# Optimization experiments

Measured on AMD Instinct MI355X. Metric: run time of the kernel, lower is better.

## Reference

```python
import jax, jax.numpy as jnp
import numpy as np

PSP_SIZES = (1, 3, 6, 8)
EPS = 1e-5  # BatchNorm eps (torch default)


def _adaptive_max_pool_flat(x, s):
    # Faithful torch AdaptiveMaxPool2d: window i is [floor(i*H/s), ceil((i+1)*H/s)).
    B, C, H, W = x.shape
    hs = [int(np.floor(i * H / s)) for i in range(s)]
    he = [int(np.ceil((i + 1) * H / s)) for i in range(s)]
    ws = [int(np.floor(j * W / s)) for j in range(s)]
    we = [int(np.ceil((j + 1) * W / s)) for j in range(s)]
    cells = []
    for i in range(s):  # small static loop (s <= 8)
        for j in range(s):
            cells.append(jnp.max(x[:, :, hs[i]:he[i], ws[j]:we[j]], axis=(2, 3)))
    return jnp.stack(cells, axis=-1)  # [B, C, s*s]


def _psp(x):
    return jnp.concatenate([_adaptive_max_pool_flat(x, s) for s in PSP_SIZES], axis=-1)  # [B, C, 110]


def _conv1x1(x, w):
    # x: [B, Cin, H, W], w: [Cout, Cin]
    return jnp.einsum('bchw,oc->bohw', x, w)


def _bn(y, gamma, beta, mean, var):
    inv = jax.lax.rsqrt(var + EPS)
    return (y - mean[None, :, None, None]) * (gamma * inv)[None, :, None, None] + beta[None, :, None, None]


def setup_inputs() -> dict:
    key = jax.random.key(0)
    ks = jax.random.split(key, 4)
    B, Cin, H, W = 8, 512, 64, 64
    Ck, Cv = 256, 512
    x = jax.random.normal(ks[0], (B, Cin, H, W), dtype=jnp.float32)
    qk_w = jax.random.normal(ks[1], (Ck, Cin), dtype=jnp.float32) * 0.02
    v_w = jax.random.normal(ks[2], (Cv, Cin), dtype=jnp.float32) * 0.02
    out_w = jax.random.normal(ks[3], (Cin, Cv), dtype=jnp.float32) * 0.02
    return {
        'x': x,
        'qk_w': qk_w, 'qk_gamma': jnp.ones(Ck), 'qk_beta': jnp.zeros(Ck),
        'qk_mean': jnp.zeros(Ck), 'qk_var': jnp.ones(Ck),
        'v_w': v_w, 'v_gamma': jnp.ones(Cv), 'v_beta': jnp.zeros(Cv),
        'v_mean': jnp.zeros(Cv), 'v_var': jnp.ones(Cv),
        'out_w': out_w, 'out_gamma': jnp.ones(Cin), 'out_beta': jnp.zeros(Cin),
        'out_mean': jnp.zeros(Cin), 'out_var': jnp.ones(Cin),
    }


def reference(x, qk_w, qk_gamma, qk_beta, qk_mean, qk_var,
              v_w, v_gamma, v_beta, v_mean, v_var,
              out_w, out_gamma, out_beta, out_mean, out_var):
    B, Cin, H, W = x.shape
    Ck = qk_w.shape[0]
    Cv = v_w.shape[0]
    # query_key branch: 1x1 conv + BN + ReLU
    qk = jax.nn.relu(_bn(_conv1x1(x, qk_w), qk_gamma, qk_beta, qk_mean, qk_var))  # [B,Ck,H,W]
    # value branch: 1x1 conv + BN + ReLU
    val = jax.nn.relu(_bn(_conv1x1(x, v_w), v_gamma, v_beta, v_mean, v_var))  # [B,Cv,H,W]
    key = _psp(qk)                          # [B, Ck, S=110]
    value = _psp(val).transpose(0, 2, 1)    # [B, S, Cv]
    query = qk.reshape(B, Ck, H * W).transpose(0, 2, 1)  # [B, N, Ck]
    scores = jnp.einsum('bnc,bcs->bns', query, key) * (Ck ** -0.5)  # [B, N, S]
    scores = jax.nn.softmax(scores, axis=-1)
    y = jnp.einsum('bns,bsc->bnc', scores, value)  # [B, N, Cv]
    y = y.transpose(0, 2, 1).reshape(B, Cv, H, W)
    y = _bn(_conv1x1(y, out_w), out_gamma, out_beta, out_mean, out_var)  # no activation
    return x + y
```

## Files before the change

kernel.cpp:

```cpp
#include <hip/hip_runtime.h>
#include <math.h>

#define B_    8
#define CIN   512
#define CK    256
#define CV    512
#define HW    4096
#define S_    110
#define SP    128
#define EPS   1e-5f

typedef __attribute__((ext_vector_type(8))) short bf16x8;
typedef __attribute__((ext_vector_type(4))) short bf16x4;
typedef __attribute__((ext_vector_type(4))) float f32x4;

__device__ __forceinline__ float b2f(short s) {
    unsigned int u = ((unsigned int)(unsigned short)s) << 16;
    union { unsigned int u; float f; } c; c.u = u; return c.f;
}
__device__ __forceinline__ short f2b(float f) {
    union { float f; unsigned int u; } c; c.f = f;
    unsigned int r = (c.u + 0x7FFFu + ((c.u >> 16) & 1u)) >> 16;
    return (short)r;
}

__device__ __forceinline__ void gload_lds16(const short* g, short* l) {
    __builtin_amdgcn_global_load_lds(
        (const __attribute__((address_space(1))) void*)g,
        (__attribute__((address_space(3))) void*)l,
        16, 0, 0);
}

template<int STRIDE>
__device__ __forceinline__ void stage_tile(
    const short* __restrict__ base, short* lds, int tid, int kt)
{
    const int wv = tid >> 6, lane = tid & 63;
    #pragma unroll
    for (int q = 0; q < 4; ++q) {
        const int u = q * 256 + wv * 64 + lane;
        const int row = u >> 3;
        const int kunit = (u & 7) ^ (row & 7);
        gload_lds16(base + (size_t)row * STRIDE + kt + kunit * 8,
                    lds + (q * 256 + wv * 64) * 8);
    }
}

__device__ __forceinline__ void mfma_step(
    const short* As, const short* Bs, int wm, int wn, int l15, int l4,
    f32x4 acc[4][4])
{
    #pragma unroll
    for (int kk = 0; kk < 2; ++kk) {
        bf16x8 af[4], bfr[4];
        #pragma unroll
        for (int m = 0; m < 4; ++m) {
            int row = wm + m * 16 + l15;
            int su = (kk * 4 + l4) ^ (row & 7);
            af[m] = *(const bf16x8*)&As[row * 64 + su * 8];
        }
        #pragma unroll
        for (int n = 0; n < 4; ++n) {
            int row = wn + n * 16 + l15;
            int su = (kk * 4 + l4) ^ (row & 7);
            bfr[n] = *(const bf16x8*)&Bs[row * 64 + su * 8];
        }
        #pragma unroll
        for (int m = 0; m < 4; ++m)
            #pragma unroll
            for (int n = 0; n < 4; ++n)
                acc[m][n] = __builtin_amdgcn_mfma_f32_16x16x32_bf16(
                    af[m], bfr[n], acc[m][n], 0, 0, 0);
    }
}

template<int NK, int SA, int SB>
__device__ __forceinline__ void gemm_loop(
    const short* __restrict__ abase, const short* __restrict__ bbase,
    short* As0, short* As1, short* Bs0, short* Bs1,
    int tid, int wm, int wn, int l15, int l4, f32x4 acc[4][4])
{
    stage_tile<SA>(abase, As0, tid, 0);
    stage_tile<SB>(bbase, Bs0, tid, 0);
    __syncthreads();
    #pragma unroll
    for (int t = 0; t < NK; t += 2) {
        if (t + 1 < NK) {
            stage_tile<SA>(abase, As1, tid, (t + 1) * 64);
            stage_tile<SB>(bbase, Bs1, tid, (t + 1) * 64);
        }
        mfma_step(As0, Bs0, wm, wn, l15, l4, acc);
        __syncthreads();
        if (t + 2 < NK) {
            stage_tile<SA>(abase, As0, tid, (t + 2) * 64);
            stage_tile<SB>(bbase, Bs0, tid, (t + 2) * 64);
        }
        mfma_step(As1, Bs1, wm, wn, l15, l4, acc);
        __syncthreads();
    }
}

__global__ __launch_bounds__(256) void transpose_x_kernel(
    const float* __restrict__ x, short* __restrict__ xt)
{
    __shared__ short t[64][65];
    const int b = blockIdx.z, c0 = blockIdx.y * 64, n0 = blockIdx.x * 64;
    const int tid = threadIdx.x;
    const float* src = x + ((size_t)b * CIN + c0) * HW + n0;
    const int j = tid & 63, i0 = tid >> 6;
    #pragma unroll
    for (int q = 0; q < 16; ++q) {
        int i = i0 * 16 + q;
        t[i][j] = f2b(src[(size_t)i * HW + j]);
    }
    __syncthreads();
    short* dst = xt + ((size_t)b * HW + n0) * CIN + c0;
    const int hh = tid & 31, jb = tid >> 5;
    #pragma unroll
    for (int q = 0; q < 8; ++q) {
        int jj = jb * 8 + q;
        short2 v; v.x = t[2 * hh][jj]; v.y = t[2 * hh + 1][jj];
        *(short2*)(dst + (size_t)jj * CIN + 2 * hh) = v;
    }
}

__global__ __launch_bounds__(256) void transpose_qk_kernel(
    const short* __restrict__ qkb, short* __restrict__ qkt)
{
    __shared__ short t[64][65];
    const int b = blockIdx.z, c0 = blockIdx.y * 64, n0 = blockIdx.x * 64;
    const int tid = threadIdx.x;
    const short* src = qkb + ((size_t)b * CK + c0) * HW + n0;
    const int j = tid & 63, i0 = tid >> 6;
    #pragma unroll
    for (int q = 0; q < 16; ++q) {
        int i = i0 * 16 + q;
        t[i][j] = src[(size_t)i * HW + j];
    }
    __syncthreads();
    short* dst = qkt + ((size_t)b * HW + n0) * CK + c0;
    const int hh = tid & 31, jb = tid >> 5;
    #pragma unroll
    for (int q = 0; q < 8; ++q) {
        int jj = jb * 8 + q;
        short2 v; v.x = t[2 * hh][jj]; v.y = t[2 * hh + 1][jj];
        *(short2*)(dst + (size_t)jj * CK + 2 * hh) = v;
    }
}

__global__ __launch_bounds__(256) void convert_w_kernel(
    const float* __restrict__ qk_w, const float* __restrict__ v_w,
    const float* __restrict__ out_w, short* __restrict__ wb)
{
    const int id4 = (blockIdx.x * 256 + threadIdx.x) * 4;
    #pragma unroll
    for (int r = 0; r < 4; ++r) {
        int id = id4 + r;
        float f = (id < 131072) ? qk_w[id]
                : (id < 393216) ? v_w[id - 131072]
                                : out_w[id - 393216];
        wb[id] = f2b(f);
    }
}

template<int MODE>
__global__ __launch_bounds__(256) void gemm_mfma_kernel(
    const short* __restrict__ W, const short* __restrict__ Bt,
    const float* __restrict__ g0, const float* __restrict__ be0,
    const float* __restrict__ mu0, const float* __restrict__ va0,
    const float* __restrict__ g1, const float* __restrict__ be1,
    const float* __restrict__ mu1, const float* __restrict__ va1,
    const float* __restrict__ xres,
    short* __restrict__ o0, short* __restrict__ o1,
    float* __restrict__ of)
{
    __shared__ short As[2][128 * 64];
    __shared__ short Bs[2][128 * 64];
    const int b   = blockIdx.z;
    const int mm0 = blockIdx.y * 128, nn0 = blockIdx.x * 128;
    const int tid = threadIdx.x;
    const int lane = tid & 63, wv = tid >> 6;
    const int wm = (wv >> 1) * 64, wn = (wv & 1) * 64;
    const int l15 = lane & 15, l4 = lane >> 4;

    const short* wbase = W + (size_t)mm0 * 512;
    const short* xbase = Bt + ((size_t)b * HW + nn0) * 512;

    f32x4 acc[4][4] = {};
    gemm_loop<8, 512, 512>(wbase, xbase, As[0], As[1], Bs[0], Bs[1],
                           tid, wm, wn, l15, l4, acc);

    #pragma unroll
    for (int m = 0; m < 4; ++m) {
        #pragma unroll
        for (int i = 0; i < 4; ++i) {
            const int co = mm0 + wm + m * 16 + l4 * 4 + i;
            if (MODE == 0) {
                float sc, sh; short* dst;
                if (co < CK) {
                    sc = g0[co] * rsqrtf(va0[co] + EPS);
                    sh = be0[co] - mu0[co] * sc;
                    dst = o0 + ((size_t)b * CK + co) * HW;
                } else {
                    int cv = co - CK;
                    sc = g1[cv] * rsqrtf(va1[cv] + EPS);
                    sh = be1[cv] - mu1[cv] * sc;
                    dst = o1 + ((size_t)b * CV + cv) * HW;
                }
                #pragma unroll
                for (int n = 0; n < 4; ++n) {
                    float v = fmaxf(acc[m][n][i] * sc + sh, 0.f);
                    dst[nn0 + wn + n * 16 + l15] = f2b(v);
                }
            } else {
                float sc = g0[co] * rsqrtf(va0[co] + EPS);
                float sh = be0[co] - mu0[co] * sc;
                const float* xr = xres + ((size_t)b * CIN + co) * HW;
                float* orow = of + ((size_t)b * CIN + co) * HW;
                #pragma unroll
                for (int n = 0; n < 4; ++n) {
                    int nidx = nn0 + wn + n * 16 + l15;
                    orow[nidx] = acc[m][n][i] * sc + sh + xr[nidx];
                }
            }
        }
    }
}

__global__ __launch_bounds__(256) void psp_pool_kernel(
    const short* __restrict__ qkb, const short* __restrict__ valb,
    short* __restrict__ keyT, short* __restrict__ valueT)
{
    __shared__ float band[4][17][64];
    const int tid = threadIdx.x;
    const int lane = tid & 63, wv = tid >> 6;
    const int c = blockIdx.x * 4 + wv;
    const int b = blockIdx.y;

    const short* src = (c < CK) ? qkb + ((size_t)b * CK + c) * HW
                                : valb + ((size_t)b * CV + (c - CK)) * HW;

    const float NEG = -1e30f;
    float a0 = NEG;
    float b3[3] = {NEG, NEG, NEG};
    float c6[6] = {NEG, NEG, NEG, NEG, NEG, NEG};
    float d8[8] = {NEG, NEG, NEG, NEG, NEG, NEG, NEG, NEG};

    #pragma unroll
    for (int h = 0; h < 64; ++h) {
        float v = b2f(src[h * 64 + lane]);
        a0 = fmaxf(a0, v);
        if (h <= 21)            b3[0] = fmaxf(b3[0], v);
        if (h >= 21 && h <= 42) b3[1] = fmaxf(b3[1], v);
        if (h >= 42)            b3[2] = fmaxf(b3[2], v);
        if (h <= 10)            c6[0] = fmaxf(c6[0], v);
        if (h >= 10 && h <= 21) c6[1] = fmaxf(c6[1], v);
        if (h >= 21 && h <= 31) c6[2] = fmaxf(c6[2], v);
        if (h >= 32 && h <= 42) c6[3] = fmaxf(c6[3], v);
        if (h >= 42 && h <= 53) c6[4] = fmaxf(c6[4], v);
        if (h >= 53)            c6[5] = fmaxf(c6[5], v);
        d8[h >> 3] = fmaxf(d8[h >> 3], v);
    }

    #pragma unroll
    for (int r = 0; r < 3; ++r) band[wv][r][lane] = b3[r];
    #pragma unroll
    for (int r = 0; r < 6; ++r) band[wv][3 + r][lane] = c6[r];
    #pragma unroll
    for (int r = 0; r < 8; ++r) band[wv][9 + r][lane] = d8[r];

    #pragma unroll
    for (int off = 32; off; off >>= 1) a0 = fmaxf(a0, __shfl_xor(a0, off));

    __syncthreads();

    const int isK = (c < CK);
    const int cv = c - CK;

    if (lane == 0) {
        if (isK) keyT[((size_t)b * SP + 0) * CK + c] = f2b(a0);
        else     valueT[((size_t)b * CV + cv) * SP + 0] = f2b(a0);
    }
    {
        int i = lane >> 3, j = lane & 7;
        const float* row = band[wv][9 + i];
        float m = row[8 * j];
        #pragma unroll
        for (int k = 1; k < 8; ++k) m = fmaxf(m, row[8 * j + k]);
        int sc = 46 + lane;
        if (isK) keyT[((size_t)b * SP + sc) * CK + c] = f2b(m);
        else     valueT[((size_t)b * CV + cv) * SP + sc] = f2b(m);
    }
    if (lane < 36) {
        int i = lane / 6, j = lane - 6 * i;
        int w0 = (j * 64) / 6, w1 = ((j + 1) * 64 + 5) / 6;
        const float* row = band[wv][3 + i];
        float m = NEG;
        for (int k = w0; k < w1; ++k) m = fmaxf(m, row[k]);
        int sc = 10 + lane;
        if (isK) keyT[((size_t)b * SP + sc) * CK + c] = f2b(m);
        else     valueT[((size_t)b * CV + cv) * SP + sc] = f2b(m);
    }
    if (lane < 9) {
        int i = lane / 3, j = lane - 3 * i;
        int w0 = (j * 64) / 3, w1 = ((j + 1) * 64 + 2) / 3;
        const float* row = band[wv][i];
        float m = NEG;
        for (int k = w0; k < w1; ++k) m = fmaxf(m, row[k]);
        int sc = 1 + lane;
        if (isK) keyT[((size_t)b * SP + sc) * CK + c] = f2b(m);
        else     valueT[((size_t)b * CV + cv) * SP + sc] = f2b(m);
    }
}

__global__ __launch_bounds__(256) void attn_scores_mfma_kernel(
    const short* __restrict__ qkt, const short* __restrict__ keyT,
    short* __restrict__ P)
{
    __shared__ short As[2][128 * 64];
    __shared__ short Bs[2][128 * 64];
    __shared__ float red[2][2][128];
    const int b  = blockIdx.y;
    const int m0 = blockIdx.x * 128;
    const int tid = threadIdx.x;
    const int lane = tid & 63, wv = tid >> 6;
    const int wm = (wv >> 1) * 64, wn = (wv & 1) * 64;
    const int l15 = lane & 15, l4 = lane >> 4;

    const short* abase = qkt + ((size_t)b * HW + m0) * CK;
    const short* bbase = keyT + (size_t)b * SP * CK;

    f32x4 acc[4][4] = {};
    gemm_loop<4, CK, CK>(abase, bbase, As[0], As[1], Bs[0], Bs[1],
                         tid, wm, wn, l15, l4, acc);

    float pv[4][4][4];
    float rmax[4][4], rsum[4][4];
    #pragma unroll
    for (int m = 0; m < 4; ++m)
        #pragma unroll
        for (int i = 0; i < 4; ++i) {
            float mx = -1e30f;
            #pragma unroll
            for (int n = 0; n < 4; ++n) {
                int s = wn + n * 16 + l15;
                float v = acc[m][n][i] * 0.0625f;
                if (s >= S_) v = -1e30f;
                pv[m][n][i] = v;
                mx = fmaxf(mx, v);
            }
            rmax[m][i] = mx;
        }
    #pragma unroll
    for (int off = 1; off < 16; off <<= 1)
        #pragma unroll
        for (int m = 0; m < 4; ++m)
            #pragma unroll
            for (int i = 0; i < 4; ++i)
                rmax[m][i] = fmaxf(rmax[m][i], __shfl_xor(rmax[m][i], off));
    if (l15 == 0) {
        #pragma unroll
        for (int m = 0; m < 4; ++m)
            #pragma unroll
            for (int i = 0; i < 4; ++i)
                red[0][wv & 1][wm + m * 16 + l4 * 4 + i] = rmax[m][i];
    }
    __syncthreads();
    #pragma unroll
    for (int m = 0; m < 4; ++m)
        #pragma unroll
        for (int i = 0; i < 4; ++i) {
            float gmax = fmaxf(rmax[m][i], red[0][(wv & 1) ^ 1][wm + m * 16 + l4 * 4 + i]);
            float sm = 0.f;
            #pragma unroll
            for (int n = 0; n < 4; ++n) {
                float e = __expf(pv[m][n][i] - gmax);
                pv[m][n][i] = e;
                sm += e;
            }
            rsum[m][i] = sm;
        }
    #pragma unroll
    for (int off = 1; off < 16; off <<= 1)
        #pragma unroll
        for (int m = 0; m < 4; ++m)
            #pragma unroll
            for (int i = 0; i < 4; ++i)
                rsum[m][i] += __shfl_xor(rsum[m][i], off);
    if (l15 == 0) {
        #pragma unroll
        for (int m = 0; m < 4; ++m)
            #pragma unroll
            for (int i = 0; i < 4; ++i)
                red[1][wv & 1][wm + m * 16 + l4 * 4 + i] = rsum[m][i];
    }
    __syncthreads();
    #pragma unroll
    for (int m = 0; m < 4; ++m)
        #pragma unroll
        for (int i = 0; i < 4; ++i) {
            int row = wm + m * 16 + l4 * 4 + i;
            float inv = 1.f / (rsum[m][i] + red[1][(wv & 1) ^ 1][row]);
            short* dst = P + ((size_t)b * HW + m0 + row) * SP + wn + l15;
            #pragma unroll
            for (int n = 0; n < 4; ++n)
                dst[n * 16] = f2b(pv[m][n][i] * inv);
        }
}

__global__ __launch_bounds__(256) void attn_pv_mfma_kernel(
    const short* __restrict__ P, const short* __restrict__ valueT,
    short* __restrict__ Yt)
{
    __shared__ short As[2][128 * 64];
    __shared__ short Bs[2][128 * 64];
    const int b   = blockIdx.z;
    const int m0  = blockIdx.y * 128;
    const int cv0 = blockIdx.x * 128;
    const int tid = threadIdx.x;
    const int lane = tid & 63, wv = tid >> 6;
    const int wm = (wv >> 1) * 64, wn = (wv & 1) * 64;
    const int l15 = lane & 15, l4 = lane >> 4;

    const short* abase = P + ((size_t)b * HW + m0) * SP;
    const short* bbase = valueT + ((size_t)b * CV + cv0) * SP;

    f32x4 acc[4][4] = {};
    gemm_loop<2, SP, SP>(abase, bbase, As[0], As[1], Bs[0], Bs[1],
                         tid, wm, wn, l15, l4, acc);

    #pragma unroll
    for (int m = 0; m < 4; ++m)
        #pragma unroll
        for (int i = 0; i < 4; ++i) {
            int row = wm + m * 16 + l4 * 4 + i;
            short* dst = Yt + ((size_t)b * HW + m0 + row) * CV + cv0 + wn + l15;
            #pragma unroll
            for (int n = 0; n < 4; ++n)
                dst[n * 16] = f2b(acc[m][n][i]);
        }
}

extern "C" void kernel_launch(void* const* d_in, const int* in_sizes, int n_in,
                              void* d_out, int out_size, void* d_ws, size_t ws_size,
                              hipStream_t stream)
{
    const float* x        = (const float*)d_in[0];
    const float* qk_w     = (const float*)d_in[1];
    const float* qk_gamma = (const float*)d_in[2];
    const float* qk_beta  = (const float*)d_in[3];
    const float* qk_mean  = (const float*)d_in[4];
    const float* qk_var   = (const float*)d_in[5];
    const float* v_w      = (const float*)d_in[6];
    const float* v_gamma  = (const float*)d_in[7];
    const float* v_beta   = (const float*)d_in[8];
    const float* v_mean   = (const float*)d_in[9];
    const float* v_var    = (const float*)d_in[10];
    const float* out_w    = (const float*)d_in[11];
    const float* out_gamma= (const float*)d_in[12];
    const float* out_beta = (const float*)d_in[13];
    const float* out_mean = (const float*)d_in[14];
    const float* out_var  = (const float*)d_in[15];

    char* wsb = (char*)d_ws;
    short* xt     = (short*)(wsb);
    short* qkt    = xt;
    short* qkb    = (short*)(wsb + 33554432);
    short* valb   = (short*)(wsb + 50331648);
    short* Yt     = valb;
    short* keyT   = (short*)(wsb + 83886080);
    short* valueT = (short*)(wsb + 84410368);
    short* P      = (short*)(wsb + 85458944);
    short* wqkv   = (short*)(wsb + 93847552);
    short* wout   = wqkv + 393216;

    transpose_x_kernel<<<dim3(HW / 64, CIN / 64, B_), 256, 0, stream>>>(x, xt);
    convert_w_kernel<<<dim3(640), 256, 0, stream>>>(qk_w, v_w, out_w, wqkv);

    gemm_mfma_kernel<0><<<dim3(HW / 128, 6, B_), 256, 0, stream>>>(
        wqkv, xt, qk_gamma, qk_beta, qk_mean, qk_var,
        v_gamma, v_beta, v_mean, v_var,
        nullptr, qkb, valb, nullptr);

    transpose_qk_kernel<<<dim3(HW / 64, CK / 64, B_), 256, 0, stream>>>(qkb, qkt);

    psp_pool_kernel<<<dim3((CK + CV) / 4, B_), 256, 0, stream>>>(qkb, valb, keyT, valueT);

    attn_scores_mfma_kernel<<<dim3(HW / 128, B_), 256, 0, stream>>>(qkt, keyT, P);

    attn_pv_mfma_kernel<<<dim3(CV / 128, HW / 128, B_), 256, 0, stream>>>(P, valueT, Yt);

    gemm_mfma_kernel<1><<<dim3(HW / 128, 4, B_), 256, 0, stream>>>(
        wout, Yt, out_gamma, out_beta, out_mean, out_var,
        nullptr, nullptr, nullptr, nullptr,
        x, nullptr, nullptr, (float*)d_out);
}
```

Baseline: 269.8 us.

## Fuse attention score softmax and PV GEMM into one kernel keeping P in LDS

Merges the scores/softmax kernel with the probability-times-value GEMM. The normalized probabilities are written into swizzled shared memory instead of global memory, and the value tiles are streamed with double buffering to produce all output channels per block. This removes the global round trip of P and one launch. In exchange, each block does four times more PV work serially, and the grid shrinks from 1024 to 256 blocks for that stage, which lowers parallelism.

```diff
diff --git a/kernel.cpp b/kernel.cpp
--- a/kernel.cpp
+++ b/kernel.cpp
@@ -313,9 +313,9 @@
     }
 }
 
-__global__ __launch_bounds__(256) void attn_scores_mfma_kernel(
+__global__ __launch_bounds__(256) void attn_fused_kernel(
     const short* __restrict__ qkt, const short* __restrict__ keyT,
-    short* __restrict__ P)
+    const short* __restrict__ valueT, short* __restrict__ Yt)
 {
     __shared__ short As[2][128 * 64];
     __shared__ short Bs[2][128 * 64];
@@ -395,50 +395,56 @@
                 red[1][wv & 1][wm + m * 16 + l4 * 4 + i] = rsum[m][i];
     }
     __syncthreads();
+
+    short* Ps = As[wv & 1];
     #pragma unroll
     for (int m = 0; m < 4; ++m)
         #pragma unroll
         for (int i = 0; i < 4; ++i) {
             int row = wm + m * 16 + l4 * 4 + i;
             float inv = 1.f / (rsum[m][i] + red[1][(wv & 1) ^ 1][row]);
-            short* dst = P + ((size_t)b * HW + m0 + row) * SP + wn + l15;
-            #pragma unroll
-            for (int n = 0; n < 4; ++n)
-                dst[n * 16] = f2b(pv[m][n][i] * inv);
-        }
-}
-
-__global__ __launch_bounds__(256) void attn_pv_mfma_kernel(
-    const short* __restrict__ P, const short* __restrict__ valueT,
-    short* __restrict__ Yt)
-{
-    __shared__ short As[2][128 * 64];
-    __shared__ short Bs[2][128 * 64];
-    const int b   = blockIdx.z;
-    const int m0  = blockIdx.y * 128;
-    const int cv0 = blockIdx.x * 128;
-    const int tid = threadIdx.x;
-    const int lane = tid & 63, wv = tid >> 6;
-    const int wm = (wv >> 1) * 64, wn = (wv & 1) * 64;
-    const int l15 = lane & 15, l4 = lane >> 4;
-
-    const short* abase = P + ((size_t)b * HW + m0) * SP;
-    const short* bbase = valueT + ((size_t)b * CV + cv0) * SP;
-
-    f32x4 acc[4][4] = {};
-    gemm_loop<2, SP, SP>(abase, bbase, As[0], As[1], Bs[0], Bs[1],
-                         tid, wm, wn, l15, l4, acc);
-
-    #pragma unroll
-    for (int m = 0; m < 4; ++m)
-        #pragma unroll
-        for (int i = 0; i < 4; ++i) {
-            int row = wm + m * 16 + l4 * 4 + i;
-            short* dst = Yt + ((size_t)b * HW + m0 + row) * CV + cv0 + wn + l15;
-            #pragma unroll
-            for (int n = 0; n < 4; ++n)
-                dst[n * 16] = f2b(acc[m][n][i]);
-        }
+            #pragma unroll
+            for (int n = 0; n < 4; ++n) {
+                int cs = n * 16 + l15;
+                int su = (cs >> 3) ^ (row & 7);
+                Ps[row * 64 + su * 8 + (cs & 7)] = f2b(pv[m][n][i] * inv);
+            }
+        }
+    __syncthreads();
+
+    const short* vbase = valueT + (size_t)b * CV * SP;
+    stage_tile<SP>(vbase, Bs[0], tid, 0);
+    __syncthreads();
+    f32x4 acc2[4][4] = {};
+    #pragma unroll
+    for (int step = 0; step < 8; ++step) {
+        const int ct = step >> 1, k = step & 1;
+        if (step + 1 < 8) {
+            const int ct2 = (step + 1) >> 1, k2 = (step + 1) & 1;
+            stage_tile<SP>(vbase + (size_t)ct2 * 128 * SP,
+                           Bs[(step + 1) & 1], tid, k2 * 64);
+        }
+        mfma_step(As[k], Bs[step & 1], wm, wn, l15, l4, acc2);
+        if (k == 1) {
+            #pragma unroll
+            for (int m = 0; m < 4; ++m)
+                #pragma unroll
+                for (int i = 0; i < 4; ++i) {
+                    int row = wm + m * 16 + l4 * 4 + i;
+                    short* dst = Yt + ((size_t)b * HW + m0 + row) * CV
+                               + ct * 128 + wn + l15;
+                    #pragma unroll
+                    for (int n = 0; n < 4; ++n)
+                        dst[n * 16] = f2b(acc2[m][n][i]);
+                }
+            #pragma unroll
+            for (int m = 0; m < 4; ++m)
+                #pragma unroll
+                for (int n = 0; n < 4; ++n)
+                    acc2[m][n] = (f32x4){0.f, 0.f, 0.f, 0.f};
+        }
+        __syncthreads();
+    }
 }
 
 extern "C" void kernel_launch(void* const* d_in, const int* in_sizes, int n_in,
@@ -470,7 +476,6 @@
     short* Yt     = valb;
     short* keyT   = (short*)(wsb + 83886080);
     short* valueT = (short*)(wsb + 84410368);
-    short* P      = (short*)(wsb + 85458944);
     short* wqkv   = (short*)(wsb + 93847552);
     short* wout   = wqkv + 393216;
 
@@ -486,9 +491,7 @@
 
     psp_pool_kernel<<<dim3((CK + CV) / 4, B_), 256, 0, stream>>>(qkb, valb, keyT, valueT);
 
-    attn_scores_mfma_kernel<<<dim3(HW / 128, B_), 256, 0, stream>>>(qkt, keyT, P);
-
-    attn_pv_mfma_kernel<<<dim3(CV / 128, HW / 128, B_), 256, 0, stream>>>(P, valueT, Yt);
+    attn_fused_kernel<<<dim3(HW / 128, B_), 256, 0, stream>>>(qkt, keyT, valueT, Yt);
 
     gemm_mfma_kernel<1><<<dim3(HW / 128, 4, B_), 256, 0, stream>>>(
         wout, Yt, out_gamma, out_beta, out_mean, out_var,
```

After: 265.4 us. About the same (-1.6%).
